# Optimization experiments

Measured on AMD Instinct MI355X. Metric: run time of the kernel, lower is better.

The kernel has to match this reference:

```python
import jax, jax.numpy as jnp
import numpy as np

B, T, N, HOR = 64, 12, 1024, 12
D_IN, D_OUT, RNN, E, K = 1, 1, 64, 8, 3
MEM_N, MEM_D = 10, 32
DEC = RNN + MEM_D  # 96 (memory_type='local')
YCOV = 1


def setup_inputs() -> dict:
    key = jax.random.key(0)
    ks = jax.random.split(key, 12)
    s = 0.1  # xavier-ish scale for weights
    return {
        "x": jax.random.normal(ks[0], (B, T, N, D_IN), jnp.float32),
        "y_cov": jax.random.normal(ks[1], (B, HOR, N, YCOV), jnp.float32),
        "node_embeddings": jax.random.normal(ks[2], (N, E), jnp.float32),
        "enc_gate_W": jax.random.normal(ks[3], (K * (D_IN + RNN), 2 * RNN), jnp.float32) * s,
        "enc_gate_b": jnp.zeros((2 * RNN,), jnp.float32),
        "enc_up_W": jax.random.normal(ks[4], (K * (D_IN + RNN), RNN), jnp.float32) * s,
        "enc_up_b": jnp.zeros((RNN,), jnp.float32),
        "Memory": jax.random.normal(ks[5], (MEM_N, MEM_D), jnp.float32) * s,
        "Wq": jax.random.normal(ks[6], (RNN, MEM_D), jnp.float32) * s,
        "FC_E": jax.random.normal(ks[7], (MEM_D, E), jnp.float32) * s,
        "dec_gate_W": jax.random.normal(ks[8], (K * (D_OUT + YCOV + DEC), 2 * DEC), jnp.float32) * s,
        "dec_gate_b": jnp.zeros((2 * DEC,), jnp.float32),
        "dec_up_W": jax.random.normal(ks[9], (K * (D_OUT + YCOV + DEC), DEC), jnp.float32) * s,
        "dec_up_b": jnp.zeros((DEC,), jnp.float32),
        "proj_W": jax.random.normal(ks[10], (DEC, D_OUT), jnp.float32) * s,
        "proj_b": jnp.zeros((D_OUT,), jnp.float32),
    }


def _cheb_supports(S):
    # S: (N,N) soft adjacency -> stacked Chebyshev set [I, S, 2S@S_{k-1}-S_{k-2}, ...], (K,N,N)
    n = S.shape[0]
    sup = [jnp.eye(n, dtype=S.dtype), S]
    for _ in range(2, K):
        sup.append(2.0 * S @ sup[-1] - sup[-2])
    return jnp.stack(sup)


def _agcn(xin, supports, W, b):
    # xin: (B,N,C); supports: (K,N,N); W: (K*C, O)
    xg = jnp.einsum('knm,bmc->bnkc', supports, xin)  # k-major matches torch cat order
    bsz, n = xin.shape[0], xin.shape[1]
    xg = xg.reshape(bsz, n, -1)
    return xg @ W + b


def _cell(xt, state, supports, gW, gb, uW, ub, hdim):
    inp = jnp.concatenate([xt, state], axis=-1)
    z_r = jax.nn.sigmoid(_agcn(inp, supports, gW, gb))
    z, r = z_r[..., :hdim], z_r[..., hdim:]
    cand = jnp.concatenate([xt, z * state], axis=-1)
    hc = jnp.tanh(_agcn(cand, supports, uW, ub))
    return r * state + (1.0 - r) * hc


def reference(x, y_cov, node_embeddings, enc_gate_W, enc_gate_b, enc_up_W, enc_up_b,
              Memory, Wq, FC_E, dec_gate_W, dec_gate_b, dec_up_W, dec_up_b, proj_W, proj_b):
    # ---- encoder supports from static node embeddings (2D path in AGCN) ----
    S_enc = jax.nn.softmax(jax.nn.relu(node_embeddings @ node_embeddings.T), axis=1)
    sup_enc = _cheb_supports(S_enc)

    # ---- encoder: GRU-style recurrence over T timesteps (lax.scan) ----
    def enc_step(state, xt):
        h = _cell(xt, state, sup_enc, enc_gate_W, enc_gate_b, enc_up_W, enc_up_b, RNN)
        return h, None
    h0 = jnp.zeros((x.shape[0], N, RNN), x.dtype)
    h_t, _ = jax.lax.scan(enc_step, h0, jnp.swapaxes(x, 0, 1))  # final hidden (B,N,RNN)

    # ---- memory query (memory_type='local') ----
    query = h_t @ Wq                                  # (B,N,MEM_D)
    att = jax.nn.softmax(query @ Memory.T, axis=-1)   # (B,N,MEM_N)
    proto_t = att @ Memory                            # (B,N,MEM_D)
    W_E = proto_t @ FC_E                              # (B,N,E) meta node embeddings

    # ---- decoder supports from meta embeddings (3D path: einsum sums over batch) ----
    S_dec = jax.nn.softmax(jax.nn.relu(jnp.einsum('bnc,bmc->nm', W_E, W_E)), axis=1)
    sup_dec = _cheb_supports(S_dec)

    # ---- stepwise decoder with go symbol ----
    dec_h0 = jnp.concatenate([h_t, proto_t], axis=-1)  # (B,N,DEC)
    go0 = jnp.zeros((x.shape[0], N, D_OUT), x.dtype)

    def dec_step(carry, yc_t):
        go, state = carry
        xt = jnp.concatenate([go, yc_t], axis=-1)
        h = _cell(xt, state, sup_dec, dec_gate_W, dec_gate_b, dec_up_W, dec_up_b, DEC)
        go_new = h @ proj_W + proj_b
        return (go_new, h), go_new

    _, outs = jax.lax.scan(dec_step, (go0, dec_h0), jnp.swapaxes(y_cov, 0, 1))
    return jnp.swapaxes(outs, 0, 1)  # (B, horizon, N, D_OUT)
```

## Files before the change

### kernel.cpp

```cpp
#include <hip/hip_runtime.h>
#include <hip/hip_bf16.h>

constexpr int B_ = 64, T_ = 12, NN = 1024, HOR_ = 12;

typedef __attribute__((ext_vector_type(8))) short short8;
typedef __attribute__((ext_vector_type(4))) float f32x4;
typedef unsigned short ushort_t;

static __device__ inline ushort_t f2bh(float v) {
  __hip_bfloat16 h = __float2bfloat16(v);
  return *reinterpret_cast<ushort_t*>(&h);
}
static __device__ inline float bh2f(ushort_t u) {
  __hip_bfloat16 h = *reinterpret_cast<__hip_bfloat16*>(&u);
  return __bfloat162float(h);
}
static __device__ inline void split_bf16(float v, ushort_t& hi, ushort_t& lo) {
  hi = f2bh(v);
  lo = f2bh(v - bh2f(hi));
}

static __device__ inline void gload_lds16(const ushort_t* g, ushort_t* l) {
  __builtin_amdgcn_global_load_lds(
      (const __attribute__((address_space(1))) unsigned int*)g,
      (__attribute__((address_space(3))) unsigned int*)l, 16, 0, 0);
}

__global__ void gemm_nt_kernel(const float* __restrict__ A, const float* __restrict__ Bm,
                               float* __restrict__ C, int Ncol, int Kd) {
  __shared__ float As[16][68];
  __shared__ float Bs[16][68];
  const int bm = blockIdx.y * 64, bn = blockIdx.x * 64;
  const int tid = threadIdx.x;
  const int tx = tid & 15, ty = tid >> 4;
  float acc[4][4] = {};
  for (int k0 = 0; k0 < Kd; k0 += 16) {
#pragma unroll
    for (int r = 0; r < 4; ++r) {
      const int m = (tid >> 4) + r * 16;
      const int kk = tid & 15;
      const int k = k0 + kk;
      As[kk][m] = (k < Kd) ? A[(size_t)(bm + m) * Kd + k] : 0.f;
      Bs[kk][m] = (k < Kd) ? Bm[(size_t)(bn + m) * Kd + k] : 0.f;
    }
    __syncthreads();
#pragma unroll
    for (int kk = 0; kk < 16; ++kk) {
      float a[4], b[4];
#pragma unroll
      for (int i = 0; i < 4; ++i) a[i] = As[kk][ty * 4 + i];
#pragma unroll
      for (int j = 0; j < 4; ++j) b[j] = Bs[kk][tx * 4 + j];
#pragma unroll
      for (int i = 0; i < 4; ++i)
#pragma unroll
        for (int j = 0; j < 4; ++j) acc[i][j] += a[i] * b[j];
    }
    __syncthreads();
  }
#pragma unroll
  for (int i = 0; i < 4; ++i)
#pragma unroll
    for (int j = 0; j < 4; ++j)
      C[(size_t)(bm + ty * 4 + i) * Ncol + bn + tx * 4 + j] = acc[i][j];
}

__global__ void relu_softmax_kernel(float* __restrict__ S, ushort_t* __restrict__ Sh,
                                    ushort_t* __restrict__ Sl) {
  const int row = blockIdx.x;
  float* r = S + (size_t)row * NN;
  const int tid = threadIdx.x;
  float v[4];
  float mx = 0.f;
#pragma unroll
  for (int j = 0; j < 4; ++j) {
    float xv = fmaxf(r[tid + j * 256], 0.f);
    v[j] = xv;
    mx = fmaxf(mx, xv);
  }
#pragma unroll
  for (int off = 1; off < 64; off <<= 1) mx = fmaxf(mx, __shfl_xor(mx, off));
  __shared__ float sred[4];
  const int wv = tid >> 6;
  if ((tid & 63) == 0) sred[wv] = mx;
  __syncthreads();
  mx = fmaxf(fmaxf(sred[0], sred[1]), fmaxf(sred[2], sred[3]));
  __syncthreads();
  float s = 0.f;
#pragma unroll
  for (int j = 0; j < 4; ++j) { v[j] = expf(v[j] - mx); s += v[j]; }
#pragma unroll
  for (int off = 1; off < 64; off <<= 1) s += __shfl_xor(s, off);
  if ((tid & 63) == 0) sred[wv] = s;
  __syncthreads();
  s = sred[0] + sred[1] + sred[2] + sred[3];
  const float inv = 1.f / s;
#pragma unroll
  for (int j = 0; j < 4; ++j) {
    const float sv = v[j] * inv;
    const size_t e = (size_t)row * NN + tid + j * 256;
    r[tid + j * 256] = sv;
    ushort_t hi, lo;
    split_bf16(sv, hi, lo);
    Sh[e] = hi;
    Sl[e] = lo;
  }
}

__global__ void st_kernel(const float* __restrict__ S, ushort_t* __restrict__ STh,
                          ushort_t* __restrict__ STl) {
  __shared__ float tile[64][65];
  const int bx = blockIdx.x * 64, by = blockIdx.y * 64;
  const int tid = threadIdx.x;
  const int cl = tid & 63, rq = tid >> 6;
#pragma unroll
  for (int r = 0; r < 16; ++r) {
    const int rr = rq + r * 4;
    tile[rr][cl] = S[(size_t)(by + rr) * NN + bx + cl];
  }
  __syncthreads();
#pragma unroll
  for (int r = 0; r < 16; ++r) {
    const int rr = rq + r * 4;
    const float v = tile[cl][rr];
    ushort_t hi, lo;
    split_bf16(v, hi, lo);
    STh[(size_t)(bx + rr) * NN + by + cl] = hi;
    STl[(size_t)(bx + rr) * NN + by + cl] = lo;
  }
}

__global__ void cheb_mfma_kernel(const ushort_t* __restrict__ S1h,
                                 const ushort_t* __restrict__ S1l,
                                 const ushort_t* __restrict__ STh,
                                 const ushort_t* __restrict__ STl,
                                 ushort_t* __restrict__ Mh) {
  __shared__ __align__(16) ushort_t sA[2 * 32 * 64];
  __shared__ __align__(16) ushort_t sB[2 * 64 * 64];
  const int bj = blockIdx.x * 64, bn = blockIdx.y * 32;
  const int tid = threadIdx.x;
  const int w = tid >> 6, lane = tid & 63;
  const int row = lane & 15, kq = lane >> 4;
  const int srow8 = lane >> 3, sslot = lane & 7;
  f32x4 acc[2] = {};
  for (int k0 = 0; k0 < NN; k0 += 64) {
#pragma unroll
    for (int t2 = 0; t2 < 2; ++t2) {
      const int c = w + t2 * 4, p = c >> 2, i = c & 3;
      const int grow = i * 8 + srow8;
      const int gch = sslot ^ (grow & 7);
      const ushort_t* src = (p ? S1l : S1h) + (size_t)(bn + grow) * NN + k0 + gch * 8;
      gload_lds16(src, sA + p * 2048 + i * 512);
    }
#pragma unroll
    for (int t2 = 0; t2 < 4; ++t2) {
      const int c2 = w + t2 * 4, p = c2 >> 3, rb = c2 & 7;
      const int grow = rb * 8 + srow8;
      const int gch = sslot ^ (grow & 7);
      const ushort_t* src = (p ? STl : STh) + (size_t)(bj + grow) * NN + k0 + gch * 8;
      gload_lds16(src, sB + p * 4096 + rb * 512);
    }
    __syncthreads();
#pragma unroll
    for (int kk = 0; kk < 2; ++kk) {
      const int rB = w * 16 + row;
      const int chB = ((kk * 4 + kq) ^ (rB & 7)) * 8;
      const short8 bh = *(const short8*)(sB + rB * 64 + chB);
      const short8 bl = *(const short8*)(sB + 4096 + rB * 64 + chB);
#pragma unroll
      for (int mt = 0; mt < 2; ++mt) {
        const int rA = mt * 16 + row;
        const int chA = ((kk * 4 + kq) ^ (rA & 7)) * 8;
        const short8 ah = *(const short8*)(sA + rA * 64 + chA);
        const short8 al = *(const short8*)(sA + 2048 + rA * 64 + chA);
        acc[mt] = __builtin_amdgcn_mfma_f32_16x16x32_bf16(ah, bh, acc[mt], 0, 0, 0);
        acc[mt] = __builtin_amdgcn_mfma_f32_16x16x32_bf16(ah, bl, acc[mt], 0, 0, 0);
        acc[mt] = __builtin_amdgcn_mfma_f32_16x16x32_bf16(al, bh, acc[mt], 0, 0, 0);
      }
    }
    __syncthreads();
  }
  const int j = bj + w * 16 + row;
#pragma unroll
  for (int mt = 0; mt < 2; ++mt) {
    const int node0 = bn + mt * 16 + kq * 4;
#pragma unroll
    for (int r = 0; r < 4; ++r)
      Mh[(size_t)(node0 + r) * NN + j] = f2bh(2.f * acc[mt][r]);
  }
}

__global__ void we_syrk_kernel(const ushort_t* __restrict__ WEh,
                               const ushort_t* __restrict__ WEl,
                               float* __restrict__ S1out) {
  __shared__ __align__(16) ushort_t sA[2 * 32 * 64];
  __shared__ __align__(16) ushort_t sB[2 * 64 * 64];
  const int bj = blockIdx.x * 64, bn = blockIdx.y * 32;
  const int tid = threadIdx.x;
  const int w = tid >> 6, lane = tid & 63;
  const int row = lane & 15, kq = lane >> 4;
  const int srow8 = lane >> 3, sslot = lane & 7;
  f32x4 acc[2] = {};
  for (int k0 = 0; k0 < 512; k0 += 64) {
#pragma unroll
    for (int t2 = 0; t2 < 6; ++t2) {
      const int cid = w + t2 * 4;
      if (cid < 8) {
        const int p = cid >> 2, i = cid & 3;
        const int grow = i * 8 + srow8;
        const int gch = sslot ^ (grow & 7);
        const ushort_t* src = (p ? WEl : WEh) + (size_t)(bn + grow) * 512 + k0 + gch * 8;
        gload_lds16(src, sA + p * 2048 + i * 512);
      } else {
        const int c2 = cid - 8, p = c2 >> 3, rb = c2 & 7;
        const int grow = rb * 8 + srow8;
        const int gch = sslot ^ (grow & 7);
        const ushort_t* src = (p ? WEl : WEh) + (size_t)(bj + grow) * 512 + k0 + gch * 8;
        gload_lds16(src, sB + p * 4096 + rb * 512);
      }
    }
    __syncthreads();
#pragma unroll
    for (int kk = 0; kk < 2; ++kk) {
      const int rB = w * 16 + row;
      const int chB = ((kk * 4 + kq) ^ (rB & 7)) * 8;
      const short8 bh = *(const short8*)(sB + rB * 64 + chB);
      const short8 bl = *(const short8*)(sB + 4096 + rB * 64 + chB);
#pragma unroll
      for (int mt = 0; mt < 2; ++mt) {
        const int rA = mt * 16 + row;
        const int chA = ((kk * 4 + kq) ^ (rA & 7)) * 8;
        const short8 ah = *(const short8*)(sA + rA * 64 + chA);
        const short8 al = *(const short8*)(sA + 2048 + rA * 64 + chA);
        acc[mt] = __builtin_amdgcn_mfma_f32_16x16x32_bf16(ah, bh, acc[mt], 0, 0, 0);
        acc[mt] = __builtin_amdgcn_mfma_f32_16x16x32_bf16(ah, bl, acc[mt], 0, 0, 0);
        acc[mt] = __builtin_amdgcn_mfma_f32_16x16x32_bf16(al, bh, acc[mt], 0, 0, 0);
      }
    }
    __syncthreads();
  }
  const int j = bj + w * 16 + row;
#pragma unroll
  for (int mt = 0; mt < 2; ++mt) {
    const int node0 = bn + mt * 16 + kq * 4;
#pragma unroll
    for (int r = 0; r < 4; ++r)
      S1out[(size_t)(node0 + r) * NN + j] = acc[mt][r];
  }
}

__global__ void wt_kernel(const float* __restrict__ W, ushort_t* __restrict__ Wth,
                          int KK, int NO, int KP, int NOP) {
  const int e = blockIdx.x * 256 + threadIdx.x;
  if (e >= NOP * KP) return;
  const int no = e / KP, k = e - no * KP;
  const float v = (no < NO && k < KK) ? W[(size_t)k * NO + no] : 0.f;
  Wth[e] = f2bh(v);
}

template <int C, int KP, int MODE>
__global__ void prep_kernel(const float* __restrict__ src0, const float* __restrict__ src1,
                            const float* __restrict__ hst,
                            ushort_t* __restrict__ Agh, ushort_t* __restrict__ XTh) {
  __shared__ float tile[64][65];
  const int bj = blockIdx.x * 64, bn = blockIdx.y * 64;
  const int tid = threadIdx.x;
  const int jl = tid & 63, nq = tid >> 6;
  const int j = bj + jl;
  const int b = j / C, c = j - b * C;
#pragma unroll
  for (int r = 0; r < 16; ++r) {
    const int node = bn + nq + r * 4;
    const int idx = node * 64 + b;
    float v;
    if (MODE == 0) {
      v = (c == 0) ? src0[((size_t)b * T_) * NN + node]
                   : hst[(size_t)idx * 64 + (c - 1)];
    } else {
      v = (c == 0) ? src0[idx]
        : (c == 1) ? src1[((size_t)b * HOR_) * NN + node]
                   : hst[(size_t)idx * 96 + (c - 2)];
    }
    tile[nq + r * 4][jl] = v;
    Agh[(size_t)idx * KP + c] = f2bh(v);
  }
  __syncthreads();
  const int nl = tid & 63, jq = tid >> 6;
#pragma unroll
  for (int r = 0; r < 16; ++r) {
    const int jj = bj + jq + r * 4;
    XTh[(size_t)jj * NN + bn + nl] = f2bh(tile[nl][jq + r * 4]);
  }
}

template <int C, int KP, bool WITHX>
__global__ void xt_kernel(ushort_t* __restrict__ Agh, ushort_t* __restrict__ XTh,
                          const float* __restrict__ x, int t) {
  __shared__ ushort_t tile[64][70];
  const int bj = blockIdx.x * 64, bn = blockIdx.y * 64;
  const int tid = threadIdx.x;
  const int jl = tid & 63, nq = tid >> 6;
  const int j = bj + jl;
  const int b = j / C, c = j - b * C;
#pragma unroll
  for (int r = 0; r < 16; ++r) {
    const int node = bn + nq + r * 4;
    const int idx = node * 64 + b;
    ushort_t uv;
    if (WITHX && c == 0) {
      uv = f2bh(x[((size_t)b * T_ + t) * NN + node]);
      Agh[(size_t)idx * KP] = uv;
    } else {
      uv = Agh[(size_t)idx * KP + c];
    }
    tile[nq + r * 4][jl] = uv;
  }
  __syncthreads();
  const int nl = tid & 63, jq = tid >> 6;
#pragma unroll
  for (int r = 0; r < 16; ++r) {
    const int jj = bj + jq + r * 4;
    XTh[(size_t)jj * NN + bn + nl] = tile[nl][jq + r * 4];
  }
}

template <int C, int KP>
__global__ void graph_mfma_kernel(const ushort_t* __restrict__ S1h,
                                  const ushort_t* __restrict__ Mh,
                                  const ushort_t* __restrict__ XTh,
                                  ushort_t* __restrict__ Agh) {
  constexpr int W = B_ * C;
  const int bj = blockIdx.x * 128;
  if (bj >= W) return;
  __shared__ __align__(16) ushort_t sA[2 * 32 * 64];
  __shared__ __align__(16) ushort_t sB[128 * 64];
  const int bn = blockIdx.y * 32;
  const int tid = threadIdx.x;
  const int w = tid >> 6, lane = tid & 63;
  const int row = lane & 15, kq = lane >> 4;
  const int srow8 = lane >> 3;
  const int sslot = lane & 7;

  const int s = w >> 1;
  const int jhalf = (w & 1) * 64;
  const ushort_t* A_lds = sA + s * (32 * 64);

  f32x4 acc[2][4] = {};
  for (int k0 = 0; k0 < NN; k0 += 64) {
#pragma unroll
    for (int t2 = 0; t2 < 6; ++t2) {
      const int cid = w + t2 * 4;
      if (cid < 8) {
        const int p = cid >> 2, i = cid & 3;
        const int grow = i * 8 + srow8;
        const int gch = sslot ^ (grow & 7);
        const ushort_t* g = (p ? Mh : S1h) + (size_t)(bn + grow) * NN + k0 + gch * 8;
        gload_lds16(g, sA + p * (32 * 64) + i * 512);
      } else {
        const int rb = cid - 8;
        const int brow = rb * 8 + srow8;
        const int gch = sslot ^ (brow & 7);
        const ushort_t* g = XTh + (size_t)(bj + brow) * NN + k0 + gch * 8;
        gload_lds16(g, sB + rb * 512);
      }
    }
    __syncthreads();
    short8 a[2][2];
#pragma unroll
    for (int kk = 0; kk < 2; ++kk)
#pragma unroll
      for (int mt = 0; mt < 2; ++mt) {
        const int r = mt * 16 + row;
        const int chunk = (kk * 4 + kq) ^ (r & 7);
        a[kk][mt] = *(const short8*)(A_lds + r * 64 + chunk * 8);
      }
#pragma unroll
    for (int nt = 0; nt < 4; ++nt) {
#pragma unroll
      for (int kk = 0; kk < 2; ++kk) {
        const int r = jhalf + nt * 16 + row;
        const int chunk = (kk * 4 + kq) ^ (r & 7);
        const short8 bh = *(const short8*)(sB + r * 64 + chunk * 8);
#pragma unroll
        for (int mt = 0; mt < 2; ++mt)
          acc[mt][nt] = __builtin_amdgcn_mfma_f32_16x16x32_bf16(a[kk][mt], bh, acc[mt][nt], 0, 0, 0);
      }
    }
    __syncthreads();
  }
  const int slice_off = (s + 1) * C;
#pragma unroll
  for (int nt = 0; nt < 4; ++nt) {
    const int j = bj + jhalf + nt * 16 + row;
    if (j < W) {
      const int b = j / C, c = j - b * C;
      const size_t coloff = (size_t)(slice_off + c);
#pragma unroll
      for (int mt = 0; mt < 2; ++mt) {
        const int node0 = bn + mt * 16 + kq * 4;
        float sub[4] = {0.f, 0.f, 0.f, 0.f};
        if (s == 1) {
          const ushort_t* xp = XTh + (size_t)j * NN + node0;
#pragma unroll
          for (int r = 0; r < 4; ++r) sub[r] = bh2f(xp[r]);
        }
#pragma unroll
        for (int r = 0; r < 4; ++r) {
          const size_t a2 = (size_t)((node0 + r) * 64 + b) * KP + coloff;
          Agh[a2] = f2bh(acc[mt][nt][r] - sub[r]);
        }
      }
    }
  }
}

template <int KP, int NO, int NOP, int MODE, int H, int CO>
__global__ void dense_mfma_kernel(ushort_t* __restrict__ Agh,
                                  const ushort_t* __restrict__ Wth,
                                  const float* __restrict__ bias,
                                  float* __restrict__ hstate,
                                  ushort_t* __restrict__ rbuf,
                                  const float* __restrict__ pW,
                                  const float* __restrict__ pb,
                                  const float* __restrict__ ycov,
                                  float* __restrict__ outp,
                                  float* __restrict__ go,
                                  int t) {
  constexpr int NFR = NO / 16;
  __shared__ __align__(16) ushort_t sAh[64 * 32];
  __shared__ __align__(16) ushort_t sBh[NOP * 32];
  const int row0 = blockIdx.x * 64;
  const int tid = threadIdx.x;
  const int w = tid >> 6, lane = tid & 63;
  const int col16 = lane & 15, four = lane >> 4;
  const int srow = lane >> 2;
  const int scol = ((lane & 3) ^ ((srow >> 1) & 3)) * 8;
  const int kqs = (four ^ ((col16 >> 1) & 3)) * 8;
  f32x4 acc[NFR] = {};
  for (int k0 = 0; k0 < KP; k0 += 32) {
    {
      const size_t g = (size_t)(row0 + w * 16 + srow) * KP + k0 + scol;
      gload_lds16(Agh + g, sAh + w * 512);
    }
    for (int c = w; c < NOP / 16; c += 4) {
      const size_t g = (size_t)(c * 16 + srow) * KP + k0 + scol;
      gload_lds16(Wth + g, sBh + c * 512);
    }
    __syncthreads();
    const short8 ah = *(const short8*)(sAh + (w * 16 + col16) * 32 + kqs);
#pragma unroll
    for (int nt = 0; nt < NFR; ++nt) {
      const int r = (nt * 16 + col16) * 32 + kqs;
      const short8 bh = *(const short8*)(sBh + r);
      acc[nt] = __builtin_amdgcn_mfma_f32_16x16x32_bf16(ah, bh, acc[nt], 0, 0, 0);
    }
    __syncthreads();
  }
  float pgo[4];
  if (MODE == 3) {
#pragma unroll
    for (int r = 0; r < 4; ++r) pgo[r] = 0.f;
  }
#pragma unroll
  for (int nt = 0; nt < NFR; ++nt) {
    const int col = nt * 16 + col16;
    const float bv = bias[col];
    const float pwv = (MODE == 3) ? pW[col] : 0.f;
    const int rbase = row0 + w * 16 + four * 4;
#pragma unroll
    for (int r = 0; r < 4; ++r) {
      const int row = rbase + r;
      const float v = acc[nt][r] + bv;
      if (MODE == 2) {
        const float sg = 1.f / (1.f + expf(-v));
        if (col < H) {
          const float hv = hstate[(size_t)row * H + col];
          Agh[(size_t)row * KP + CO + col] = f2bh(sg * hv);
        } else {
          rbuf[(size_t)row * H + (col - H)] = f2bh(sg);
        }
      } else {
        const float rg = bh2f(rbuf[(size_t)row * H + col]);
        const float hv = hstate[(size_t)row * H + col];
        const float hnew = rg * hv + (1.f - rg) * tanhf(v);
        hstate[(size_t)row * H + col] = hnew;
        Agh[(size_t)row * KP + CO + col] = f2bh(hnew);
        if (MODE == 3) pgo[r] += hnew * pwv;
      }
    }
  }
  if (MODE == 3) {
#pragma unroll
    for (int r = 0; r < 4; ++r) {
      float v = pgo[r];
      v += __shfl_xor(v, 1);
      v += __shfl_xor(v, 2);
      v += __shfl_xor(v, 4);
      v += __shfl_xor(v, 8);
      v += pb[0];
      if (col16 == 0) {
        const int row = row0 + w * 16 + four * 4 + r;
        const int n = row >> 6, b = row & 63;
        outp[((size_t)b * HOR_ + t) * NN + n] = v;
        go[row] = v;
        if (t + 1 < HOR_) {
          Agh[(size_t)row * KP + 0] = f2bh(v);
          Agh[(size_t)row * KP + 1] = f2bh(ycov[((size_t)b * HOR_ + t + 1) * NN + n]);
        }
      }
    }
  }
}

__global__ void attn_kernel(const float* __restrict__ h, const float* __restrict__ Wq,
                            const float* __restrict__ Mem, const float* __restrict__ FCE,
                            float* __restrict__ hB, ushort_t* __restrict__ WEh,
                            ushort_t* __restrict__ WEl) {
  __shared__ float sWq[64 * 32];
  __shared__ float sM[10 * 32];
  __shared__ float sF[32 * 8];
  const int tid = threadIdx.x;
  for (int i = tid; i < 64 * 32; i += 256) sWq[i] = Wq[i];
  for (int i = tid; i < 10 * 32; i += 256) sM[i] = Mem[i];
  for (int i = tid; i < 32 * 8; i += 256) sF[i] = FCE[i];
  __syncthreads();
  const int idx = blockIdx.x * 256 + tid;
  const float* hp = h + (size_t)idx * 64;
  float* hd = hB + (size_t)idx * 96;
  float q[32] = {};
  for (int i0 = 0; i0 < 16; ++i0) {
    const float4 h4 = *(const float4*)(hp + i0 * 4);
#pragma unroll
    for (int jj = 0; jj < 4; ++jj) {
      const float hv = ((const float*)&h4)[jj];
      hd[i0 * 4 + jj] = hv;
      const int i = i0 * 4 + jj;
#pragma unroll
      for (int c = 0; c < 32; ++c) q[c] += hv * sWq[i * 32 + c];
    }
  }
  float lg[10];
  float mx = -1e30f;
#pragma unroll
  for (int m = 0; m < 10; ++m) {
    float s = 0.f;
#pragma unroll
    for (int c = 0; c < 32; ++c) s += q[c] * sM[m * 32 + c];
    lg[m] = s;
    mx = fmaxf(mx, s);
  }
  float den = 0.f;
#pragma unroll
  for (int m = 0; m < 10; ++m) { lg[m] = expf(lg[m] - mx); den += lg[m]; }
  const float inv = 1.f / den;
  float p[32] = {};
#pragma unroll
  for (int m = 0; m < 10; ++m) {
    const float a = lg[m] * inv;
#pragma unroll
    for (int c = 0; c < 32; ++c) p[c] += a * sM[m * 32 + c];
  }
#pragma unroll
  for (int c = 0; c < 32; ++c) hd[64 + c] = p[c];
#pragma unroll
  for (int e = 0; e < 8; ++e) {
    float s = 0.f;
#pragma unroll
    for (int c = 0; c < 32; ++c) s += p[c] * sF[c * 8 + e];
    ushort_t hi, lo;
    split_bf16(s, hi, lo);
    WEh[(size_t)idx * 8 + e] = hi;
    WEl[(size_t)idx * 8 + e] = lo;
  }
}

extern "C" void kernel_launch(void* const* d_in, const int* in_sizes, int n_in,
                              void* d_out, int out_size, void* d_ws, size_t ws_size,
                              hipStream_t stream) {
  const float* x    = (const float*)d_in[0];
  const float* ycov = (const float*)d_in[1];
  const float* emb  = (const float*)d_in[2];
  const float* egW  = (const float*)d_in[3];
  const float* egb  = (const float*)d_in[4];
  const float* euW  = (const float*)d_in[5];
  const float* eub  = (const float*)d_in[6];
  const float* Mem  = (const float*)d_in[7];
  const float* Wq   = (const float*)d_in[8];
  const float* FCE  = (const float*)d_in[9];
  const float* dgW  = (const float*)d_in[10];
  const float* dgb  = (const float*)d_in[11];
  const float* duW  = (const float*)d_in[12];
  const float* dub  = (const float*)d_in[13];
  const float* pW   = (const float*)d_in[14];
  const float* pb   = (const float*)d_in[15];
  float* out = (float*)d_out;

  char* w = (char*)d_ws;
  auto alloc = [&](size_t bytes) {
    void* p = (void*)w;
    w += (bytes + 255) & ~(size_t)255;
    return p;
  };
  float* S1   = (float*)alloc((size_t)NN * NN * 4);
  float* hA   = (float*)alloc((size_t)NN * B_ * 64 * 4);
  float* hB   = (float*)alloc((size_t)NN * B_ * 96 * 4);
  float* go   = (float*)alloc((size_t)NN * B_ * 4);
  ushort_t* rbuf = (ushort_t*)alloc((size_t)NN * B_ * 96 * 2);
  ushort_t* WEh = (ushort_t*)alloc((size_t)NN * 512 * 2);
  ushort_t* WEl = (ushort_t*)alloc((size_t)NN * 512 * 2);
  ushort_t* S1h = (ushort_t*)alloc((size_t)NN * NN * 2);
  ushort_t* S1l = (ushort_t*)alloc((size_t)NN * NN * 2);
  ushort_t* Mh  = (ushort_t*)alloc((size_t)NN * NN * 2);
  ushort_t* STh = (ushort_t*)alloc((size_t)NN * NN * 2);
  ushort_t* STl = (ushort_t*)alloc((size_t)NN * NN * 2);
  ushort_t* XTh = (ushort_t*)alloc((size_t)B_ * 98 * NN * 2);
  ushort_t* Agh = (ushort_t*)alloc((size_t)NN * B_ * 320 * 2);
  ushort_t* WtegH = (ushort_t*)alloc(128 * 224 * 2);
  ushort_t* WteuH = (ushort_t*)alloc(64 * 224 * 2);
  ushort_t* WtdgH = (ushort_t*)alloc(192 * 320 * 2);
  ushort_t* WtduH = (ushort_t*)alloc(128 * 320 * 2);
  (void)ws_size; (void)in_sizes; (void)n_in; (void)out_size;

  const dim3 blk(256);

  wt_kernel<<<(128 * 224 + 255) / 256, blk, 0, stream>>>(egW, WtegH, 195, 128, 224, 128);
  wt_kernel<<<(64 * 224 + 255) / 256, blk, 0, stream>>>(euW, WteuH, 195, 64, 224, 64);
  wt_kernel<<<(192 * 320 + 255) / 256, blk, 0, stream>>>(dgW, WtdgH, 294, 192, 320, 192);
  wt_kernel<<<(128 * 320 + 255) / 256, blk, 0, stream>>>(duW, WtduH, 294, 96, 320, 128);
  hipMemsetAsync(Agh, 0, (size_t)NN * B_ * 320 * 2, stream);
  hipMemsetAsync(hA, 0, (size_t)NN * B_ * 64 * 4, stream);
  hipMemsetAsync(go, 0, (size_t)NN * B_ * 4, stream);

  gemm_nt_kernel<<<dim3(16, 16), blk, 0, stream>>>(emb, emb, S1, NN, 8);
  relu_softmax_kernel<<<NN, blk, 0, stream>>>(S1, S1h, S1l);
  st_kernel<<<dim3(16, 16), blk, 0, stream>>>(S1, STh, STl);
  cheb_mfma_kernel<<<dim3(16, 32), blk, 0, stream>>>(S1h, S1l, STh, STl, Mh);

  for (int t = 0; t < T_; ++t) {
    if (t == 0) {
      prep_kernel<65, 224, 0><<<dim3(65, 16), blk, 0, stream>>>(x, nullptr, hA, Agh, XTh);
    } else {
      xt_kernel<65, 224, true><<<dim3(65, 16), blk, 0, stream>>>(Agh, XTh, x, t);
    }
    graph_mfma_kernel<65, 224><<<dim3(40, 32), blk, 0, stream>>>(S1h, Mh, XTh, Agh);
    dense_mfma_kernel<224, 128, 128, 2, 64, 1><<<1024, blk, 0, stream>>>(
        Agh, WtegH, egb, hA, rbuf, nullptr, nullptr, nullptr, nullptr, nullptr, 0);
    xt_kernel<65, 224, false><<<dim3(65, 16), blk, 0, stream>>>(Agh, XTh, nullptr, 0);
    graph_mfma_kernel<65, 224><<<dim3(40, 32), blk, 0, stream>>>(S1h, Mh, XTh, Agh);
    dense_mfma_kernel<224, 64, 64, 1, 64, 1><<<1024, blk, 0, stream>>>(
        Agh, WteuH, eub, hA, rbuf, nullptr, nullptr, nullptr, nullptr, nullptr, 0);
  }

  attn_kernel<<<256, blk, 0, stream>>>(hA, Wq, Mem, FCE, hB, WEh, WEl);
  we_syrk_kernel<<<dim3(16, 32), blk, 0, stream>>>(WEh, WEl, S1);
  relu_softmax_kernel<<<NN, blk, 0, stream>>>(S1, S1h, S1l);
  st_kernel<<<dim3(16, 16), blk, 0, stream>>>(S1, STh, STl);
  cheb_mfma_kernel<<<dim3(16, 32), blk, 0, stream>>>(S1h, S1l, STh, STl, Mh);

  for (int t = 0; t < HOR_; ++t) {
    if (t == 0) {
      prep_kernel<98, 320, 2><<<dim3(98, 16), blk, 0, stream>>>(go, ycov, hB, Agh, XTh);
    } else {
      xt_kernel<98, 320, false><<<dim3(98, 16), blk, 0, stream>>>(Agh, XTh, nullptr, 0);
    }
    graph_mfma_kernel<98, 320><<<dim3(56, 32), blk, 0, stream>>>(S1h, Mh, XTh, Agh);
    dense_mfma_kernel<320, 192, 192, 2, 96, 2><<<1024, blk, 0, stream>>>(
        Agh, WtdgH, dgb, hB, rbuf, nullptr, nullptr, nullptr, nullptr, nullptr, 0);
    xt_kernel<98, 320, false><<<dim3(98, 16), blk, 0, stream>>>(Agh, XTh, nullptr, 0);
    graph_mfma_kernel<98, 320><<<dim3(56, 32), blk, 0, stream>>>(S1h, Mh, XTh, Agh);
    dense_mfma_kernel<320, 96, 128, 3, 96, 2><<<1024, blk, 0, stream>>>(
        Agh, WtduH, dub, hB, rbuf, pW, pb, ycov, out, go, t);
  }
}
```

Measured before the change: 3.570 ms.

## Retile graph GEMM to 128x128 blocks with 32x32x16 MFMA and split supports across grid z

Each graph propagation block used to compute a 32-node slice for both supports (S and the Chebyshev term) using 16x16x32 MFMAs. It now computes a 128-node by 128-column tile for a single support, selected by blockIdx.z, using 32x32x16 bf16 MFMAs. Each B-tile load from XTh is reused across four times as many rows, and the larger MFMA shape needs fewer LDS fragment reads per flop. In exchange the grid has fewer, larger blocks, each holding more accumulator registers. The epilogue's scattered per-element stores and the per-element XTh subtraction reads for the Chebyshev slice remain.

After: 3.911 ms. 9.5% more time.

```diff
diff --git a/kernel.cpp b/kernel.cpp
--- a/kernel.cpp
+++ b/kernel.cpp
@@ -5,6 +5,7 @@
 
 typedef __attribute__((ext_vector_type(8))) short short8;
 typedef __attribute__((ext_vector_type(4))) float f32x4;
+typedef __attribute__((ext_vector_type(16))) float f32x16;
 typedef unsigned short ushort_t;
 
 static __device__ inline ushort_t f2bh(float v) {
@@ -332,82 +333,73 @@
   constexpr int W = B_ * C;
   const int bj = blockIdx.x * 128;
   if (bj >= W) return;
-  __shared__ __align__(16) ushort_t sA[2 * 32 * 64];
+  const int bn = blockIdx.y * 128;
+  const int s = blockIdx.z;
+  const ushort_t* Ag = s ? Mh : S1h;
+  __shared__ __align__(16) ushort_t sA[128 * 64];
   __shared__ __align__(16) ushort_t sB[128 * 64];
-  const int bn = blockIdx.y * 32;
   const int tid = threadIdx.x;
   const int w = tid >> 6, lane = tid & 63;
-  const int row = lane & 15, kq = lane >> 4;
-  const int srow8 = lane >> 3;
-  const int sslot = lane & 7;
-
-  const int s = w >> 1;
-  const int jhalf = (w & 1) * 64;
-  const ushort_t* A_lds = sA + s * (32 * 64);
-
-  f32x4 acc[2][4] = {};
+  const int srow8 = lane >> 3, sslot = lane & 7;
+  const int mrow = (w >> 1) * 64, jcol = (w & 1) * 64;
+  const int l31 = lane & 31, khalf = lane >> 5;
+
+  f32x16 acc[2][2] = {};
   for (int k0 = 0; k0 < NN; k0 += 64) {
 #pragma unroll
-    for (int t2 = 0; t2 < 6; ++t2) {
+    for (int t2 = 0; t2 < 8; ++t2) {
       const int cid = w + t2 * 4;
-      if (cid < 8) {
-        const int p = cid >> 2, i = cid & 3;
-        const int grow = i * 8 + srow8;
+      if (cid < 16) {
+        const int grow = cid * 8 + srow8;
         const int gch = sslot ^ (grow & 7);
-        const ushort_t* g = (p ? Mh : S1h) + (size_t)(bn + grow) * NN + k0 + gch * 8;
-        gload_lds16(g, sA + p * (32 * 64) + i * 512);
+        gload_lds16(Ag + (size_t)(bn + grow) * NN + k0 + gch * 8, sA + cid * 512);
       } else {
-        const int rb = cid - 8;
+        const int rb = cid - 16;
         const int brow = rb * 8 + srow8;
         const int gch = sslot ^ (brow & 7);
-        const ushort_t* g = XTh + (size_t)(bj + brow) * NN + k0 + gch * 8;
-        gload_lds16(g, sB + rb * 512);
-      }
-    }
-    __syncthreads();
-    short8 a[2][2];
-#pragma unroll
-    for (int kk = 0; kk < 2; ++kk)
+        gload_lds16(XTh + (size_t)(bj + brow) * NN + k0 + gch * 8, sB + rb * 512);
+      }
+    }
+    __syncthreads();
+#pragma unroll
+    for (int kk = 0; kk < 4; ++kk) {
+      short8 a[2], b[2];
 #pragma unroll
       for (int mt = 0; mt < 2; ++mt) {
-        const int r = mt * 16 + row;
-        const int chunk = (kk * 4 + kq) ^ (r & 7);
-        a[kk][mt] = *(const short8*)(A_lds + r * 64 + chunk * 8);
-      }
-#pragma unroll
-    for (int nt = 0; nt < 4; ++nt) {
-#pragma unroll
-      for (int kk = 0; kk < 2; ++kk) {
-        const int r = jhalf + nt * 16 + row;
-        const int chunk = (kk * 4 + kq) ^ (r & 7);
-        const short8 bh = *(const short8*)(sB + r * 64 + chunk * 8);
-#pragma unroll
-        for (int mt = 0; mt < 2; ++mt)
-          acc[mt][nt] = __builtin_amdgcn_mfma_f32_16x16x32_bf16(a[kk][mt], bh, acc[mt][nt], 0, 0, 0);
-      }
+        const int r = mrow + mt * 32 + l31;
+        const int ch = (kk * 2 + khalf) ^ (r & 7);
+        a[mt] = *(const short8*)(sA + r * 64 + ch * 8);
+      }
+#pragma unroll
+      for (int nt = 0; nt < 2; ++nt) {
+        const int r = jcol + nt * 32 + l31;
+        const int ch = (kk * 2 + khalf) ^ (r & 7);
+        b[nt] = *(const short8*)(sB + r * 64 + ch * 8);
+      }
+#pragma unroll
+      for (int mt = 0; mt < 2; ++mt)
+#pragma unroll
+        for (int nt = 0; nt < 2; ++nt)
+          acc[mt][nt] = __builtin_amdgcn_mfma_f32_32x32x16_bf16(a[mt], b[nt], acc[mt][nt], 0, 0, 0);
     }
     __syncthreads();
   }
   const int slice_off = (s + 1) * C;
 #pragma unroll
-  for (int nt = 0; nt < 4; ++nt) {
-    const int j = bj + jhalf + nt * 16 + row;
+  for (int nt = 0; nt < 2; ++nt) {
+    const int j = bj + jcol + nt * 32 + l31;
     if (j < W) {
       const int b = j / C, c = j - b * C;
       const size_t coloff = (size_t)(slice_off + c);
 #pragma unroll
       for (int mt = 0; mt < 2; ++mt) {
-        const int node0 = bn + mt * 16 + kq * 4;
-        float sub[4] = {0.f, 0.f, 0.f, 0.f};
-        if (s == 1) {
-          const ushort_t* xp = XTh + (size_t)j * NN + node0;
-#pragma unroll
-          for (int r = 0; r < 4; ++r) sub[r] = bh2f(xp[r]);
-        }
-#pragma unroll
-        for (int r = 0; r < 4; ++r) {
-          const size_t a2 = (size_t)((node0 + r) * 64 + b) * KP + coloff;
-          Agh[a2] = f2bh(acc[mt][nt][r] - sub[r]);
+#pragma unroll
+        for (int reg = 0; reg < 16; ++reg) {
+          const int row32 = (reg & 3) + 8 * (reg >> 2) + 4 * khalf;
+          const int node = bn + mrow + mt * 32 + row32;
+          float v = acc[mt][nt][reg];
+          if (s == 1) v -= bh2f(XTh[(size_t)j * NN + node]);
+          Agh[(size_t)(node * 64 + b) * KP + coloff] = f2bh(v);
         }
       }
     }
@@ -642,11 +634,11 @@
     } else {
       xt_kernel<65, 224, true><<<dim3(65, 16), blk, 0, stream>>>(Agh, XTh, x, t);
     }
-    graph_mfma_kernel<65, 224><<<dim3(40, 32), blk, 0, stream>>>(S1h, Mh, XTh, Agh);
+    graph_mfma_kernel<65, 224><<<dim3(40, 8, 2), blk, 0, stream>>>(S1h, Mh, XTh, Agh);
     dense_mfma_kernel<224, 128, 128, 2, 64, 1><<<1024, blk, 0, stream>>>(
         Agh, WtegH, egb, hA, rbuf, nullptr, nullptr, nullptr, nullptr, nullptr, 0);
     xt_kernel<65, 224, false><<<dim3(65, 16), blk, 0, stream>>>(Agh, XTh, nullptr, 0);
-    graph_mfma_kernel<65, 224><<<dim3(40, 32), blk, 0, stream>>>(S1h, Mh, XTh, Agh);
+    graph_mfma_kernel<65, 224><<<dim3(40, 8, 2), blk, 0, stream>>>(S1h, Mh, XTh, Agh);
     dense_mfma_kernel<224, 64, 64, 1, 64, 1><<<1024, blk, 0, stream>>>(
         Agh, WteuH, eub, hA, rbuf, nullptr, nullptr, nullptr, nullptr, nullptr, 0);
   }
@@ -663,11 +655,11 @@
     } else {
       xt_kernel<98, 320, false><<<dim3(98, 16), blk, 0, stream>>>(Agh, XTh, nullptr, 0);
     }
-    graph_mfma_kernel<98, 320><<<dim3(56, 32), blk, 0, stream>>>(S1h, Mh, XTh, Agh);
+    graph_mfma_kernel<98, 320><<<dim3(56, 8, 2), blk, 0, stream>>>(S1h, Mh, XTh, Agh);
     dense_mfma_kernel<320, 192, 192, 2, 96, 2><<<1024, blk, 0, stream>>>(
         Agh, WtdgH, dgb, hB, rbuf, nullptr, nullptr, nullptr, nullptr, nullptr, 0);
     xt_kernel<98, 320, false><<<dim3(98, 16), blk, 0, stream>>>(Agh, XTh, nullptr, 0);
-    graph_mfma_kernel<98, 320><<<dim3(56, 32), blk, 0, stream>>>(S1h, Mh, XTh, Agh);
+    graph_mfma_kernel<98, 320><<<dim3(56, 8, 2), blk, 0, stream>>>(S1h, Mh, XTh, Agh);
     dense_mfma_kernel<320, 96, 128, 3, 96, 2><<<1024, blk, 0, stream>>>(
         Agh, WtduH, dub, hB, rbuf, pW, pb, ycov, out, go, t);
   }
```
